# Kernel tuning notes

Hardware: AMD Instinct MI355X
Metric: run time of the kernel (lower is better)

The kernel has to match this reference:

```python
import jax, jax.numpy as jnp
import numpy as np

D_MODEL = 768
D_STATE = 16
D_CONV = 4
EXPAND = 2
D_INNER = D_MODEL * EXPAND  # 1536
B = 2
T = 8192
ALPHA = 0.9  # hard-coded EMA coefficient in _parallel_scan


def setup_inputs() -> dict:
    key = jax.random.key(0)
    ks = jax.random.split(key, 12)
    s = 0.02
    return {
        "x": jax.random.normal(ks[0], (B, T, D_MODEL), jnp.float32),
        "in_w": jax.random.normal(ks[1], (D_MODEL, 2 * D_INNER), jnp.float32) * s,
        "in_b": jnp.zeros((2 * D_INNER,), jnp.float32),
        "conv_w": jax.random.normal(ks[2], (D_INNER, 1, D_CONV), jnp.float32) * s,  # OIH, depthwise
        "conv_b": jnp.zeros((D_INNER,), jnp.float32),
        "xp_w": jax.random.normal(ks[3], (D_INNER, 2 * D_STATE), jnp.float32) * s,
        "xp_b": jnp.zeros((2 * D_STATE,), jnp.float32),
        "dt_w": jax.random.normal(ks[4], (D_STATE, D_INNER), jnp.float32) * s,
        "dt_b": jnp.zeros((D_INNER,), jnp.float32),
        "D_param": jnp.ones((D_INNER,), jnp.float32),
        "out_w": jax.random.normal(ks[5], (D_INNER, D_MODEL), jnp.float32) * s,
        "out_b": jnp.zeros((D_MODEL,), jnp.float32),
    }


def _forward(x, in_w, in_b, conv_w, conv_b, xp_w, xp_b, dt_w, dt_b, D_param, out_w, out_b):
    # in_proj: [B,T,D] -> [B,T,2*d_inner]
    xz = x @ in_w + in_b
    x_inner, z = jnp.split(xz, 2, axis=-1)

    # Causal depthwise conv1d (torch pads both sides by d_conv-1 then slices [:T],
    # which is equivalent to left-pad d_conv-1, right-pad 0)
    xc = jnp.transpose(x_inner, (0, 2, 1))  # [B, d_inner, T]
    xc = jax.lax.conv_general_dilated(
        xc, conv_w, window_strides=(1,), padding=[(D_CONV - 1, 0)],
        dimension_numbers=("NCH", "OIH", "NCH"), feature_group_count=D_INNER,
    ) + conv_b[None, :, None]
    x_conv = jax.nn.silu(jnp.transpose(xc, (0, 2, 1)))  # [B, T, d_inner]

    # NOTE: original computes x_proj/dt_proj/A_bar here, but _parallel_scan ignores
    # A_bar/B_ssm/C_ssm entirely, so they are dead code w.r.t. the output (omitted).

    # Serial EMA scan: h_t = alpha*h_{t-1} + (1-alpha)*x_conv_t
    def step(h, xt):
        h = ALPHA * h + (1.0 - ALPHA) * xt
        return h, h

    h0 = jnp.zeros((x.shape[0], D_INNER), x_conv.dtype)
    _, hs = jax.lax.scan(step, h0, jnp.transpose(x_conv, (1, 0, 2)))  # [T,B,d_inner]
    scan_out = jnp.transpose(hs, (1, 0, 2))

    y = x_conv * D_param + scan_out
    y = y * jax.nn.silu(z)
    return y @ out_w + out_b  # dropout is identity at inference


def reference(x, in_w, in_b, conv_w, conv_b, xp_w, xp_b, dt_w, dt_b, D_param, out_w, out_b):
    return _forward(x, in_w, in_b, conv_w, conv_b, xp_w, xp_b, dt_w, dt_b, D_param, out_w, out_b)
```

## Files before the change

### kernel.cpp

```cpp
#include <hip/hip_runtime.h>

#define D_MODEL 768
#define D_INNER 1536
#define NXZ     3072
#define BATCH   2
#define SEQ     8192
#define MTOT    (BATCH*SEQ)
#define CHUNK   128
#define WARM    64

typedef _Float16 v8h __attribute__((ext_vector_type(8)));
typedef _Float16 v4h __attribute__((ext_vector_type(4)));
typedef float    v4f __attribute__((ext_vector_type(4)));
typedef _Float16 f16;

__global__ void k_cvt(const float* __restrict__ in, f16* __restrict__ out, int n4) {
  int i = blockIdx.x * blockDim.x + threadIdx.x;
  if (i < n4) {
    float4 v = reinterpret_cast<const float4*>(in)[i];
    v4h o;
    o[0] = (f16)v.x; o[1] = (f16)v.y; o[2] = (f16)v.z; o[3] = (f16)v.w;
    reinterpret_cast<v4h*>(out)[i] = o;
  }
}

__global__ void k_transpose_cvt(const float* __restrict__ in, f16* __restrict__ out,
                                int R, int C) {
  __shared__ float tile[32][33];
  int c0 = blockIdx.x * 32, r0 = blockIdx.y * 32;
  int tx = threadIdx.x, ty = threadIdx.y;
#pragma unroll
  for (int i = 0; i < 32; i += 8)
    tile[ty + i][tx] = in[(long)(r0 + ty + i) * C + (c0 + tx)];
  __syncthreads();
#pragma unroll
  for (int i = 0; i < 32; i += 8)
    out[(long)(c0 + ty + i) * R + (r0 + tx)] = (f16)tile[tx][ty + i];
}

__device__ __forceinline__ void gload_lds16(const void* g, void* l) {
  __builtin_amdgcn_global_load_lds((const __attribute__((address_space(1))) void*)g,
                                   (__attribute__((address_space(3))) void*)l, 16, 0, 0);
}

template <bool F16OUT>
__launch_bounds__(256, 2)
__global__ void k_gemm_bt(const f16* __restrict__ A, const f16* __restrict__ Bt,
                          const float* __restrict__ bias, void* __restrict__ Cv,
                          int M, int N, int K) {
  __shared__ f16 As[128][32];
  __shared__ f16 Bs[128][32];
  const int tid  = threadIdx.x;
  const int lane = tid & 63;
  const int wave = tid >> 6;
  const int wm   = (wave >> 1) * 64;
  const int wn   = (wave & 1) * 64;
  const int m16  = lane & 15;
  const int quad = lane >> 4;
  const long m0 = (long)blockIdx.y * 128;
  const long n0 = (long)blockIdx.x * 128;

  v4f acc[4][4];
#pragma unroll
  for (int i = 0; i < 4; i++)
#pragma unroll
    for (int j = 0; j < 4; j++)
#pragma unroll
      for (int r = 0; r < 4; r++) acc[i][j][r] = 0.f;

  const int srow = wave * 16 + (lane >> 2);
  const int scol = (lane & 3) * 8;
  const f16* Ag = A  + (m0 + srow) * (long)K + scol;
  const f16* Bg = Bt + (n0 + srow) * (long)K + scol;
  f16* AsW0 = &As[wave * 16][0];
  f16* AsW1 = &As[64 + wave * 16][0];
  f16* BsW0 = &Bs[wave * 16][0];
  f16* BsW1 = &Bs[64 + wave * 16][0];

  for (int k0 = 0; k0 < K; k0 += 32) {
    gload_lds16(Ag,                 AsW0);
    gload_lds16(Ag + (long)64 * K,  AsW1);
    gload_lds16(Bg,                 BsW0);
    gload_lds16(Bg + (long)64 * K,  BsW1);
    Ag += 32; Bg += 32;
    __syncthreads();
    v8h af[4], bfr[4];
#pragma unroll
    for (int i = 0; i < 4; i++) af[i]  = *(const v8h*)&As[wm + i * 16 + m16][quad * 8];
#pragma unroll
    for (int j = 0; j < 4; j++) bfr[j] = *(const v8h*)&Bs[wn + j * 16 + m16][quad * 8];
#pragma unroll
    for (int i = 0; i < 4; i++)
#pragma unroll
      for (int j = 0; j < 4; j++)
        acc[i][j] = __builtin_amdgcn_mfma_f32_16x16x32_f16(af[i], bfr[j], acc[i][j], 0, 0, 0);
    __syncthreads();
  }

#pragma unroll
  for (int i = 0; i < 4; i++) {
#pragma unroll
    for (int j = 0; j < 4; j++) {
      const long n = n0 + wn + j * 16 + m16;
      const float bv = bias[n];
#pragma unroll
      for (int r = 0; r < 4; r++) {
        const long m = m0 + wm + i * 16 + quad * 4 + r;
        float v = acc[i][j][r] + bv;
        if (F16OUT) ((f16*)Cv)[m * N + n] = (f16)v;
        else        ((float*)Cv)[m * N + n] = v;
      }
    }
  }
}

__global__ void k_conv_scan(const f16* __restrict__ xz, const float* __restrict__ conv_w,
                            const float* __restrict__ conv_b, const float* __restrict__ Dp_,
                            f16* __restrict__ y) {
  const int c  = blockIdx.y * 256 + threadIdx.x;
  const int b  = blockIdx.z;
  const int t0 = blockIdx.x * CHUNK;
  const float w0 = conv_w[c * 4 + 0], w1 = conv_w[c * 4 + 1];
  const float w2 = conv_w[c * 4 + 2], w3 = conv_w[c * 4 + 3];
  const float cb = conv_b[c], Dp = Dp_[c];
  const f16* xin = xz + (long)b * SEQ * NXZ + c;
  const f16* zin = xin + D_INNER;
  f16* yout = y + (long)b * SEQ * D_INNER + c;

  int ts = t0 - WARM; if (ts < 0) ts = 0;
  float xm3 = (ts >= 3) ? (float)xin[(long)(ts - 3) * NXZ] : 0.f;
  float xm2 = (ts >= 2) ? (float)xin[(long)(ts - 2) * NXZ] : 0.f;
  float xm1 = (ts >= 1) ? (float)xin[(long)(ts - 1) * NXZ] : 0.f;
  float h = 0.f;

#pragma unroll 4
  for (int t = ts; t < t0; ++t) {
    float xt = (float)xin[(long)t * NXZ];
    float u = w0 * xm3 + w1 * xm2 + w2 * xm1 + w3 * xt + cb;
    float v = u / (1.f + __expf(-u));
    h = 0.9f * h + 0.1f * v;
    xm3 = xm2; xm2 = xm1; xm1 = xt;
  }
  const int tend = t0 + CHUNK;
#pragma unroll 4
  for (int t = t0; t < tend; ++t) {
    float xt = (float)xin[(long)t * NXZ];
    float u = w0 * xm3 + w1 * xm2 + w2 * xm1 + w3 * xt + cb;
    float v = u / (1.f + __expf(-u));
    h = 0.9f * h + 0.1f * v;
    float zv = (float)zin[(long)t * NXZ];
    float g = zv / (1.f + __expf(-zv));
    yout[(long)t * D_INNER] = (f16)((v * Dp + h) * g);
    xm3 = xm2; xm2 = xm1; xm1 = xt;
  }
}

extern "C" void kernel_launch(void* const* d_in, const int* in_sizes, int n_in,
                              void* d_out, int out_size, void* d_ws, size_t ws_size,
                              hipStream_t stream) {
  const float* x       = (const float*)d_in[0];
  const float* in_w    = (const float*)d_in[1];
  const float* in_b    = (const float*)d_in[2];
  const float* conv_w  = (const float*)d_in[3];
  const float* conv_b  = (const float*)d_in[4];
  const float* D_param = (const float*)d_in[9];
  const float* out_w   = (const float*)d_in[10];
  const float* out_b   = (const float*)d_in[11];
  float* out = (float*)d_out;

  char* p = (char*)d_ws;
  f16* xb    = (f16*)p; p += (size_t)MTOT * D_MODEL * 2;
  f16* wInT  = (f16*)p; p += (size_t)NXZ * D_MODEL * 2;
  f16* wOutT = (f16*)p; p += (size_t)D_MODEL * D_INNER * 2;
  f16* xzb   = (f16*)p; p += (size_t)MTOT * NXZ * 2;
  f16* yb    = (f16*)p; p += (size_t)MTOT * D_INNER * 2;

  k_cvt<<<(MTOT * D_MODEL / 4 + 255) / 256, 256, 0, stream>>>(x, xb, MTOT * D_MODEL / 4);
  k_transpose_cvt<<<dim3(NXZ / 32, D_MODEL / 32), dim3(32, 8), 0, stream>>>(in_w, wInT, D_MODEL, NXZ);
  k_transpose_cvt<<<dim3(D_MODEL / 32, D_INNER / 32), dim3(32, 8), 0, stream>>>(out_w, wOutT, D_INNER, D_MODEL);

  k_gemm_bt<true><<<dim3(NXZ / 128, MTOT / 128), 256, 0, stream>>>(xb, wInT, in_b, xzb, MTOT, NXZ, D_MODEL);

  k_conv_scan<<<dim3(SEQ / CHUNK, D_INNER / 256, BATCH), 256, 0, stream>>>(xzb, conv_w, conv_b, D_param, yb);

  k_gemm_bt<false><<<dim3(D_MODEL / 128, MTOT / 128), 256, 0, stream>>>(yb, wOutT, out_b, out, MTOT, D_MODEL, D_INNER);
}
```

Before: 352.4 us.

## Store in-proj output transposed and swizzle GEMM LDS tiles

The first GEMM now writes xz transposed (channel-major, time contiguous) with packed 4-wide f16 stores. The conv/scan kernel reads 8 timesteps per vector load instead of strided per-step loads. Separately, the LDS tile columns are XOR-swizzled on both the global-to-LDS write and the fragment read, to reduce bank conflicts. The transposed layout makes the scan's per-thread loads strided across threads (one row per channel), which may hurt coalescing.

Result: slower. 421.1 us (+19.5%).

```diff
diff --git a/kernel.cpp b/kernel.cpp
--- a/kernel.cpp
+++ b/kernel.cpp
@@ -43,7 +43,7 @@
                                    (__attribute__((address_space(3))) void*)l, 16, 0, 0);
 }
 
-template <bool F16OUT>
+template <int OUT_MODE>
 __launch_bounds__(256, 2)
 __global__ void k_gemm_bt(const f16* __restrict__ A, const f16* __restrict__ Bt,
                           const float* __restrict__ bias, void* __restrict__ Cv,
@@ -57,6 +57,7 @@
   const int wn   = (wave & 1) * 64;
   const int m16  = lane & 15;
   const int quad = lane >> 4;
+  const int rsw  = (m16 >> 1) & 3;
   const long m0 = (long)blockIdx.y * 128;
   const long n0 = (long)blockIdx.x * 128;
 
@@ -69,7 +70,7 @@
       for (int r = 0; r < 4; r++) acc[i][j][r] = 0.f;
 
   const int srow = wave * 16 + (lane >> 2);
-  const int scol = (lane & 3) * 8;
+  const int scol = (((lane & 3) ^ ((lane >> 3) & 3)) << 3);
   const f16* Ag = A  + (m0 + srow) * (long)K + scol;
   const f16* Bg = Bt + (n0 + srow) * (long)K + scol;
   f16* AsW0 = &As[wave * 16][0];
@@ -86,9 +87,9 @@
     __syncthreads();
     v8h af[4], bfr[4];
 #pragma unroll
-    for (int i = 0; i < 4; i++) af[i]  = *(const v8h*)&As[wm + i * 16 + m16][quad * 8];
-#pragma unroll
-    for (int j = 0; j < 4; j++) bfr[j] = *(const v8h*)&Bs[wn + j * 16 + m16][quad * 8];
+    for (int i = 0; i < 4; i++) af[i]  = *(const v8h*)&As[wm + i * 16 + m16][(quad ^ rsw) * 8];
+#pragma unroll
+    for (int j = 0; j < 4; j++) bfr[j] = *(const v8h*)&Bs[wn + j * 16 + m16][(quad ^ rsw) * 8];
 #pragma unroll
     for (int i = 0; i < 4; i++)
 #pragma unroll
@@ -97,24 +98,39 @@
     __syncthreads();
   }
 
-#pragma unroll
-  for (int i = 0; i < 4; i++) {
-#pragma unroll
-    for (int j = 0; j < 4; j++) {
-      const long n = n0 + wn + j * 16 + m16;
-      const float bv = bias[n];
-#pragma unroll
-      for (int r = 0; r < 4; r++) {
-        const long m = m0 + wm + i * 16 + quad * 4 + r;
-        float v = acc[i][j][r] + bv;
-        if (F16OUT) ((f16*)Cv)[m * N + n] = (f16)v;
-        else        ((float*)Cv)[m * N + n] = v;
+  if (OUT_MODE == 1) {
+    f16* Ct = (f16*)Cv;
+#pragma unroll
+    for (int i = 0; i < 4; i++) {
+#pragma unroll
+      for (int j = 0; j < 4; j++) {
+        const long n = n0 + wn + j * 16 + m16;
+        const float bv = bias[n];
+        v4h pk;
+#pragma unroll
+        for (int r = 0; r < 4; r++) pk[r] = (f16)(acc[i][j][r] + bv);
+        *(v4h*)&Ct[n * (long)M + (m0 + wm + i * 16 + quad * 4)] = pk;
       }
     }
-  }
-}
-
-__global__ void k_conv_scan(const f16* __restrict__ xz, const float* __restrict__ conv_w,
+  } else {
+    float* C = (float*)Cv;
+#pragma unroll
+    for (int i = 0; i < 4; i++) {
+#pragma unroll
+      for (int j = 0; j < 4; j++) {
+        const long n = n0 + wn + j * 16 + m16;
+        const float bv = bias[n];
+#pragma unroll
+        for (int r = 0; r < 4; r++) {
+          const long m = m0 + wm + i * 16 + quad * 4 + r;
+          C[m * N + n] = acc[i][j][r] + bv;
+        }
+      }
+    }
+  }
+}
+
+__global__ void k_conv_scan(const f16* __restrict__ xzT, const float* __restrict__ conv_w,
                             const float* __restrict__ conv_b, const float* __restrict__ Dp_,
                             f16* __restrict__ y) {
   const int c  = blockIdx.y * 256 + threadIdx.x;
@@ -123,35 +139,40 @@
   const float w0 = conv_w[c * 4 + 0], w1 = conv_w[c * 4 + 1];
   const float w2 = conv_w[c * 4 + 2], w3 = conv_w[c * 4 + 3];
   const float cb = conv_b[c], Dp = Dp_[c];
-  const f16* xin = xz + (long)b * SEQ * NXZ + c;
-  const f16* zin = xin + D_INNER;
+  const f16* xr = xzT + (long)c * MTOT + (long)b * SEQ;
+  const f16* zr = xzT + (long)(c + D_INNER) * MTOT + (long)b * SEQ;
   f16* yout = y + (long)b * SEQ * D_INNER + c;
 
-  int ts = t0 - WARM; if (ts < 0) ts = 0;
-  float xm3 = (ts >= 3) ? (float)xin[(long)(ts - 3) * NXZ] : 0.f;
-  float xm2 = (ts >= 2) ? (float)xin[(long)(ts - 2) * NXZ] : 0.f;
-  float xm1 = (ts >= 1) ? (float)xin[(long)(ts - 1) * NXZ] : 0.f;
+  const int ts = (t0 >= WARM) ? (t0 - WARM) : 0;
+  float xm3 = 0.f, xm2 = 0.f, xm1 = 0.f;
+  if (ts >= 3) { xm3 = (float)xr[ts - 3]; xm2 = (float)xr[ts - 2]; xm1 = (float)xr[ts - 1]; }
   float h = 0.f;
 
-#pragma unroll 4
-  for (int t = ts; t < t0; ++t) {
-    float xt = (float)xin[(long)t * NXZ];
-    float u = w0 * xm3 + w1 * xm2 + w2 * xm1 + w3 * xt + cb;
-    float v = u / (1.f + __expf(-u));
-    h = 0.9f * h + 0.1f * v;
-    xm3 = xm2; xm2 = xm1; xm1 = xt;
-  }
-  const int tend = t0 + CHUNK;
-#pragma unroll 4
-  for (int t = t0; t < tend; ++t) {
-    float xt = (float)xin[(long)t * NXZ];
-    float u = w0 * xm3 + w1 * xm2 + w2 * xm1 + w3 * xt + cb;
-    float v = u / (1.f + __expf(-u));
-    h = 0.9f * h + 0.1f * v;
-    float zv = (float)zin[(long)t * NXZ];
-    float g = zv / (1.f + __expf(-zv));
-    yout[(long)t * D_INNER] = (f16)((v * Dp + h) * g);
-    xm3 = xm2; xm2 = xm1; xm1 = xt;
+  for (int t8 = ts; t8 < t0; t8 += 8) {
+    v8h xv = *(const v8h*)&xr[t8];
+#pragma unroll
+    for (int k = 0; k < 8; k++) {
+      float xt = (float)xv[k];
+      float u = w0 * xm3 + w1 * xm2 + w2 * xm1 + w3 * xt + cb;
+      float v = u / (1.f + __expf(-u));
+      h = 0.9f * h + 0.1f * v;
+      xm3 = xm2; xm2 = xm1; xm1 = xt;
+    }
+  }
+  for (int t8 = t0; t8 < t0 + CHUNK; t8 += 8) {
+    v8h xv = *(const v8h*)&xr[t8];
+    v8h zv8 = *(const v8h*)&zr[t8];
+#pragma unroll
+    for (int k = 0; k < 8; k++) {
+      float xt = (float)xv[k];
+      float u = w0 * xm3 + w1 * xm2 + w2 * xm1 + w3 * xt + cb;
+      float v = u / (1.f + __expf(-u));
+      h = 0.9f * h + 0.1f * v;
+      float zv = (float)zv8[k];
+      float g = zv / (1.f + __expf(-zv));
+      yout[(long)(t8 + k) * D_INNER] = (f16)((v * Dp + h) * g);
+      xm3 = xm2; xm2 = xm1; xm1 = xt;
+    }
   }
 }
 
@@ -172,16 +193,16 @@
   f16* xb    = (f16*)p; p += (size_t)MTOT * D_MODEL * 2;
   f16* wInT  = (f16*)p; p += (size_t)NXZ * D_MODEL * 2;
   f16* wOutT = (f16*)p; p += (size_t)D_MODEL * D_INNER * 2;
-  f16* xzb   = (f16*)p; p += (size_t)MTOT * NXZ * 2;
+  f16* xzT   = (f16*)p; p += (size_t)MTOT * NXZ * 2;
   f16* yb    = (f16*)p; p += (size_t)MTOT * D_INNER * 2;
 
   k_cvt<<<(MTOT * D_MODEL / 4 + 255) / 256, 256, 0, stream>>>(x, xb, MTOT * D_MODEL / 4);
   k_transpose_cvt<<<dim3(NXZ / 32, D_MODEL / 32), dim3(32, 8), 0, stream>>>(in_w, wInT, D_MODEL, NXZ);
   k_transpose_cvt<<<dim3(D_MODEL / 32, D_INNER / 32), dim3(32, 8), 0, stream>>>(out_w, wOutT, D_INNER, D_MODEL);
 
-  k_gemm_bt<true><<<dim3(NXZ / 128, MTOT / 128), 256, 0, stream>>>(xb, wInT, in_b, xzb, MTOT, NXZ, D_MODEL);
-
-  k_conv_scan<<<dim3(SEQ / CHUNK, D_INNER / 256, BATCH), 256, 0, stream>>>(xzb, conv_w, conv_b, D_param, yb);
-
-  k_gemm_bt<false><<<dim3(D_MODEL / 128, MTOT / 128), 256, 0, stream>>>(yb, wOutT, out_b, out, MTOT, D_MODEL, D_INNER);
-}
+  k_gemm_bt<1><<<dim3(NXZ / 128, MTOT / 128), 256, 0, stream>>>(xb, wInT, in_b, xzT, MTOT, NXZ, D_MODEL);
+
+  k_conv_scan<<<dim3(SEQ / CHUNK, D_INNER / 256, BATCH), 256, 0, stream>>>(xzT, conv_w, conv_b, D_param, yb);
+
+  k_gemm_bt<0><<<dim3(D_MODEL / 128, MTOT / 128), 256, 0, stream>>>(yb, wOutT, out_b, out, MTOT, D_MODEL, D_INNER);
+}
```

## Swizzle GEMM LDS layout and stage conv-scan inputs through shared memory

Applied to the files above, without the earlier changes.

Adds an XOR swizzle to the LDS column index in the GEMM, applied both where global_load_lds writes and where the MFMA fragments are read, to cut LDS bank conflicts. Rewrites the conv+scan kernel to load 64-timestep tiles of x and z cooperatively into shared memory with 16-byte vector loads, then run the serial recurrence per channel from LDS. This replaces the strided 2-byte per-thread global loads. It adds two block syncs per tile and 64 KB of LDS per block, which may limit occupancy.

Result: no change. 348.3 us (-1.1%).

```diff
diff --git a/kernel.cpp b/kernel.cpp
--- a/kernel.cpp
+++ b/kernel.cpp
@@ -6,7 +6,6 @@
 #define BATCH   2
 #define SEQ     8192
 #define MTOT    (BATCH*SEQ)
-#define CHUNK   128
 #define WARM    64
 
 typedef _Float16 v8h __attribute__((ext_vector_type(8)));
@@ -57,6 +56,7 @@
   const int wn   = (wave & 1) * 64;
   const int m16  = lane & 15;
   const int quad = lane >> 4;
+  const int rsw  = (m16 >> 1) & 3;
   const long m0 = (long)blockIdx.y * 128;
   const long n0 = (long)blockIdx.x * 128;
 
@@ -69,7 +69,7 @@
       for (int r = 0; r < 4; r++) acc[i][j][r] = 0.f;
 
   const int srow = wave * 16 + (lane >> 2);
-  const int scol = (lane & 3) * 8;
+  const int scol = (((lane & 3) ^ ((lane >> 3) & 3)) << 3);
   const f16* Ag = A  + (m0 + srow) * (long)K + scol;
   const f16* Bg = Bt + (n0 + srow) * (long)K + scol;
   f16* AsW0 = &As[wave * 16][0];
@@ -86,9 +86,9 @@
     __syncthreads();
     v8h af[4], bfr[4];
 #pragma unroll
-    for (int i = 0; i < 4; i++) af[i]  = *(const v8h*)&As[wm + i * 16 + m16][quad * 8];
-#pragma unroll
-    for (int j = 0; j < 4; j++) bfr[j] = *(const v8h*)&Bs[wn + j * 16 + m16][quad * 8];
+    for (int i = 0; i < 4; i++) af[i]  = *(const v8h*)&As[wm + i * 16 + m16][(quad ^ rsw) * 8];
+#pragma unroll
+    for (int j = 0; j < 4; j++) bfr[j] = *(const v8h*)&Bs[wn + j * 16 + m16][(quad ^ rsw) * 8];
 #pragma unroll
     for (int i = 0; i < 4; i++)
 #pragma unroll
@@ -117,41 +117,65 @@
 __global__ void k_conv_scan(const f16* __restrict__ xz, const float* __restrict__ conv_w,
                             const float* __restrict__ conv_b, const float* __restrict__ Dp_,
                             f16* __restrict__ y) {
-  const int c  = blockIdx.y * 256 + threadIdx.x;
-  const int b  = blockIdx.z;
-  const int t0 = blockIdx.x * CHUNK;
+  __shared__ f16 xs[64][256];
+  __shared__ f16 zs[64][256];
+  const int tid = threadIdx.x;
+  const int c0  = blockIdx.y * 256;
+  const int c   = c0 + tid;
+  const int b   = blockIdx.z;
+  const int t0  = blockIdx.x * 128;
   const float w0 = conv_w[c * 4 + 0], w1 = conv_w[c * 4 + 1];
   const float w2 = conv_w[c * 4 + 2], w3 = conv_w[c * 4 + 3];
   const float cb = conv_b[c], Dp = Dp_[c];
-  const f16* xin = xz + (long)b * SEQ * NXZ + c;
-  const f16* zin = xin + D_INNER;
-  f16* yout = y + (long)b * SEQ * D_INNER + c;
-
-  int ts = t0 - WARM; if (ts < 0) ts = 0;
-  float xm3 = (ts >= 3) ? (float)xin[(long)(ts - 3) * NXZ] : 0.f;
-  float xm2 = (ts >= 2) ? (float)xin[(long)(ts - 2) * NXZ] : 0.f;
-  float xm1 = (ts >= 1) ? (float)xin[(long)(ts - 1) * NXZ] : 0.f;
-  float h = 0.f;
-
-#pragma unroll 4
-  for (int t = ts; t < t0; ++t) {
-    float xt = (float)xin[(long)t * NXZ];
-    float u = w0 * xm3 + w1 * xm2 + w2 * xm1 + w3 * xt + cb;
-    float v = u / (1.f + __expf(-u));
-    h = 0.9f * h + 0.1f * v;
-    xm3 = xm2; xm2 = xm1; xm1 = xt;
-  }
-  const int tend = t0 + CHUNK;
-#pragma unroll 4
-  for (int t = t0; t < tend; ++t) {
-    float xt = (float)xin[(long)t * NXZ];
-    float u = w0 * xm3 + w1 * xm2 + w2 * xm1 + w3 * xt + cb;
-    float v = u / (1.f + __expf(-u));
-    h = 0.9f * h + 0.1f * v;
-    float zv = (float)zin[(long)t * NXZ];
-    float g = zv / (1.f + __expf(-zv));
-    yout[(long)t * D_INNER] = (f16)((v * Dp + h) * g);
-    xm3 = xm2; xm2 = xm1; xm1 = xt;
+  const long mb = (long)b * SEQ;
+
+  float xm3 = 0.f, xm2 = 0.f, xm1 = 0.f, h = 0.f;
+  const int ts = t0 - WARM;
+  if (t0 > 0) {
+    xm3 = (float)xz[(mb + ts - 3) * (long)NXZ + c];
+    xm2 = (float)xz[(mb + ts - 2) * (long)NXZ + c];
+    xm1 = (float)xz[(mb + ts - 1) * (long)NXZ + c];
+  }
+
+  for (int p = 0; p < 3; ++p) {
+    const int tp = ts + p * 64;
+    __syncthreads();
+    if (tp >= 0) {
+#pragma unroll
+      for (int j = 0; j < 8; ++j) {
+        const int idx = j * 256 + tid, row = idx >> 5, col = (idx & 31) << 3;
+        *(v8h*)&xs[row][col] = *(const v8h*)&xz[(mb + tp + row) * (long)NXZ + c0 + col];
+      }
+      if (p > 0) {
+#pragma unroll
+        for (int j = 0; j < 8; ++j) {
+          const int idx = j * 256 + tid, row = idx >> 5, col = (idx & 31) << 3;
+          *(v8h*)&zs[row][col] = *(const v8h*)&xz[(mb + tp + row) * (long)NXZ + D_INNER + c0 + col];
+        }
+      }
+    }
+    __syncthreads();
+    if (tp < 0) continue;
+    if (p == 0) {
+      for (int tl = 0; tl < 64; ++tl) {
+        float xt = (float)xs[tl][tid];
+        float u = w0 * xm3 + w1 * xm2 + w2 * xm1 + w3 * xt + cb;
+        h = 0.9f * h + 0.1f * (u / (1.f + __expf(-u)));
+        xm3 = xm2; xm2 = xm1; xm1 = xt;
+      }
+    } else {
+      f16* yo = y + (mb + tp) * (long)D_INNER + c;
+      for (int tl = 0; tl < 64; ++tl) {
+        float xt = (float)xs[tl][tid];
+        float u = w0 * xm3 + w1 * xm2 + w2 * xm1 + w3 * xt + cb;
+        float v = u / (1.f + __expf(-u));
+        h = 0.9f * h + 0.1f * v;
+        float zv = (float)zs[tl][tid];
+        float g = zv / (1.f + __expf(-zv));
+        yo[(long)tl * D_INNER] = (f16)((v * Dp + h) * g);
+        xm3 = xm2; xm2 = xm1; xm1 = xt;
+      }
+    }
   }
 }
 
@@ -181,7 +205,7 @@
 
   k_gemm_bt<true><<<dim3(NXZ / 128, MTOT / 128), 256, 0, stream>>>(xb, wInT, in_b, xzb, MTOT, NXZ, D_MODEL);
 
-  k_conv_scan<<<dim3(SEQ / CHUNK, D_INNER / 256, BATCH), 256, 0, stream>>>(xzb, conv_w, conv_b, D_param, yb);
+  k_conv_scan<<<dim3(SEQ / 128, D_INNER / 256, BATCH), 256, 0, stream>>>(xzb, conv_w, conv_b, D_param, yb);
 
   k_gemm_bt<false><<<dim3(D_MODEL / 128, MTOT / 128), 256, 0, stream>>>(yb, wOutT, out_b, out, MTOT, D_MODEL, D_INNER);
 }
```
